# Kernel tuning notes

Measured on AMD Instinct MI355X. Metric: run time of the kernel, lower is better.

The kernel has to match this reference:

```python
import jax, jax.numpy as jnp
import numpy as np

N = 32768          # total proposals (batch of images concatenated)
C = 81             # num classes (class 0 = background)
K = 4096           # fixed candidate budget for masked NMS (jit-friendly)
SCORE_THRESH = 0.05
NMS_THRESH = 0.5
IMG_W, IMG_H = 1333.0, 800.0   # image size for clip_to_image
CLS_OFFSET = 4096.0            # > max coord: offsets boxes per label so NMS is per-class


def setup_inputs() -> dict:
    key = jax.random.key(0)
    k1, k2, k3 = jax.random.split(key, 3)
    x = jax.random.normal(k1, (N, C), dtype=jnp.float32)
    xy = jax.random.uniform(k2, (N, 2), dtype=jnp.float32) * jnp.array([IMG_W * 0.9, IMG_H * 0.9], jnp.float32)
    wh = 4.0 + jax.random.uniform(k3, (N, 2), dtype=jnp.float32) * 124.0
    boxes = jnp.concatenate([xy, xy + wh], axis=-1)  # [N,4] xyxy
    return {"x": x, "boxes": boxes}


def _pairwise_iou(b):
    # b: [K,4] xyxy -> [K,K] IoU
    x1, y1, x2, y2 = b[:, 0], b[:, 1], b[:, 2], b[:, 3]
    area = (x2 - x1) * (y2 - y1)
    iw = jnp.maximum(jnp.minimum(x2[:, None], x2[None, :]) - jnp.maximum(x1[:, None], x1[None, :]), 0.0)
    ih = jnp.maximum(jnp.minimum(y2[:, None], y2[None, :]) - jnp.maximum(y1[:, None], y1[None, :]), 0.0)
    inter = iw * ih
    return inter / (area[:, None] + area[None, :] - inter + 1e-9)


def reference(x, boxes):
    # softmax scores
    prob = jax.nn.softmax(x, axis=-1)                    # [N,C]
    # clip_to_image (remove_empty=False)
    bx = jnp.stack([
        jnp.clip(boxes[:, 0], 0.0, IMG_W - 1),
        jnp.clip(boxes[:, 1], 0.0, IMG_H - 1),
        jnp.clip(boxes[:, 2], 0.0, IMG_W - 1),
        jnp.clip(boxes[:, 3], 0.0, IMG_H - 1)], axis=-1)  # [N,4]
    # score threshold + drop background (label 0), as in filter_results
    valid = (prob > SCORE_THRESH) & (jnp.arange(C)[None, :] != 0)
    flat = jnp.where(valid, prob, -1.0).reshape(-1)       # [N*C]
    vals, idx = jax.lax.top_k(flat, K)                    # sorted desc
    box_idx = idx // C
    labels = idx % C                                      # [K] int
    bk = bx[box_idx]                                      # [K,4] (boxes repeated per class in torch code)
    keep0 = vals > 0.0                                    # invalid slots padded with -1
    # multi-label NMS: offset boxes by label so different classes never overlap
    boff = bk + (labels.astype(bk.dtype) * CLS_OFFSET)[:, None]
    iou_gt = _pairwise_iou(boff) > NMS_THRESH             # [K,K] bool
    order = jnp.arange(K)

    def step(keep, i):
        sup = keep[i] & (order > i) & iou_gt[i]
        return keep & ~sup, None

    keep, _ = jax.lax.scan(step, keep0, order)
    dets = jnp.where(keep[:, None],
                     jnp.concatenate([bk, vals[:, None]], axis=-1),
                     0.0)                                 # [K,5] = xyxy + score
    return dets, labels, keep
```

## Files before the change

kernel.cpp:

```cpp
#include <hip/hip_runtime.h>

#pragma clang fp contract(off)

typedef unsigned int u32;
typedef unsigned long long u64;
typedef long long i64;

#define N_ROWS 32768
#define NCLS 81
#define TOPK 4096
#define IMGW_M1 1332.0f
#define IMGH_M1 799.0f

#define CAND_THREADS 256
#define RPB 32
#define CAND_GRID (N_ROWS / RPB)
#define CPT 11
#define BLK_CAND_CAP 640
#define ROW_F4 ((RPB * NCLS) / 4)

#define H1_BASE 0x3D4Cu
#define H1_BINS 576

#define NSLICE 32
#define SUBCAP 384
#define SEG_LDS 4096

#define MCAP 1024
#define MMAX 512
#define NW32 16

__device__ inline double fast_exp_neg(double d) {
    if (d < -45.0) return 0.0;
    const double L2E    = 1.4426950408889634074;
    const double LN2_HI = 6.93147180369123816490e-01;
    const double LN2_LO = 1.90821492927058770002e-10;
    double n = __builtin_rint(d * L2E);
    double r = __builtin_fma(-n, LN2_HI, d);
    r = __builtin_fma(-n, LN2_LO, r);
    double p = 1.0 / 6227020800.0;
    p = __builtin_fma(p, r, 1.0 / 479001600.0);
    p = __builtin_fma(p, r, 1.0 / 39916800.0);
    p = __builtin_fma(p, r, 1.0 / 3628800.0);
    p = __builtin_fma(p, r, 1.0 / 362880.0);
    p = __builtin_fma(p, r, 1.0 / 40320.0);
    p = __builtin_fma(p, r, 1.0 / 5040.0);
    p = __builtin_fma(p, r, 1.0 / 720.0);
    p = __builtin_fma(p, r, 1.0 / 120.0);
    p = __builtin_fma(p, r, 1.0 / 24.0);
    p = __builtin_fma(p, r, 1.0 / 6.0);
    p = __builtin_fma(p, r, 0.5);
    p = __builtin_fma(p, r, 1.0);
    p = __builtin_fma(p, r, 1.0);
    i64 ni = (i64)n;
    double sc = __longlong_as_double((i64)(1023 + ni) << 52);
    return p * sc;
}

__global__ void __launch_bounds__(256) k_cand(const float* __restrict__ x,
                                              u32* __restrict__ binCur,
                                              u64* __restrict__ selBins) {
    __shared__ float4 lx4[ROW_F4];
    __shared__ u32 lK[BLK_CAND_CAP];
    __shared__ u32 lI[BLK_CAND_CAP];
    __shared__ u32 lcnt;
    float* lx = (float*)lx4;
    const int t = threadIdx.x;
    if (t == 0) lcnt = 0;

    const float4* xv = (const float4*)x + (size_t)blockIdx.x * ROW_F4;
    for (int i = t; i < ROW_F4; i += CAND_THREADS) lx4[i] = xv[i];
    __syncthreads();

    const int rl = t >> 3;
    const int q = t & 7;
    const int c0 = q * 10;
    const int cEff = (q == 7) ? 11 : 10;
    const int row = blockIdx.x * RPB + rl;
    const float* xr = lx + rl * NCLS;

    float v[CPT];
    #pragma unroll
    for (int i = 0; i < CPT; i++) v[i] = (i < cEff) ? xr[c0 + i] : -1.0e30f;

    float m = v[0];
    #pragma unroll
    for (int i = 1; i < CPT; i++) m = fmaxf(m, v[i]);
    m = fmaxf(m, __shfl_xor(m, 1));
    m = fmaxf(m, __shfl_xor(m, 2));
    m = fmaxf(m, __shfl_xor(m, 4));

    double e[CPT];
    #pragma unroll
    for (int i = 0; i < CPT; i++) {
        if (i < cEff) {
            float d = v[i] - m;
            e[i] = fast_exp_neg((double)d);
        } else e[i] = 0.0;
    }
    double s = 0.0;
    #pragma unroll
    for (int i = 0; i < CPT; i++) if (i < cEff) s += e[i];
    s += __shfl_xor(s, 1);
    s += __shfl_xor(s, 2);
    s += __shfl_xor(s, 4);

    const double THRMID = (double)0.05f + 0x1.0p-29;
    double ethr = THRMID * s;
    #pragma unroll
    for (int i = 0; i < CPT; i++) {
        int c = c0 + i;
        if (i < cEff && c != 0 && e[i] > ethr) {
            float pf = (float)(e[i] / s);
            u32 slot = atomicAdd(&lcnt, 1u);
            lK[slot] = __float_as_uint(pf);
            lI[slot] = (u32)(row * NCLS + c);
        }
    }
    __syncthreads();

    const u32 tot = lcnt;
    const u32 sbase = (blockIdx.x & (NSLICE - 1)) * H1_BINS;
    for (u32 i = t; i < tot; i += CAND_THREADS) {
        u32 key = lK[i];
        u32 b = (key >> 16) - H1_BASE;
        u32 pos = atomicAdd(&binCur[sbase + b], 1u);
        if (pos < (u32)SUBCAP)
            selBins[(size_t)(sbase + b) * SUBCAP + pos] =
                ((u64)key << 32) | (u64)(0xFFFFFFFFu - lI[i]);
    }
}

__global__ void __launch_bounds__(256) k_binrank(const u64* __restrict__ selBins,
                                                 const u32* __restrict__ binCur,
                                                 const float* __restrict__ boxes,
                                                 float* __restrict__ rboxes,
                                                 float* __restrict__ rvals,
                                                 int* __restrict__ rlabel,
                                                 float* __restrict__ out) {
    __shared__ u32 cs[1040];
    __shared__ u64 seg[SEG_LDS];
    __shared__ u32 sBase[NSLICE + 1];
    __shared__ u32 Bsh;
    const int t = threadIdx.x;

    if (t == 0) Bsh = 0;

    {
        u32 s0 = 0, s1 = 0, s2 = 0;
        const bool g1 = (t + 256) < H1_BINS;
        const bool g2 = (t + 512) < H1_BINS;
        #pragma unroll 4
        for (int j = 0; j < NSLICE; j++) {
            const u32* hp = binCur + j * H1_BINS;
            s0 += hp[t];
            if (g1) s1 += hp[t + 256];
            if (g2) s2 += hp[t + 512];
        }
        cs[t] = s0;
        cs[t + 256] = g1 ? s1 : 0u;
        cs[t + 512] = g2 ? s2 : 0u;
        cs[t + 768] = 0u;
    }
    __syncthreads();
    for (int d = 1; d < 1024; d <<= 1) {
        u32 a0 = (t + d < 1024) ? cs[t + d] : 0u;
        u32 a1 = (t + 256 + d < 1024) ? cs[t + 256 + d] : 0u;
        u32 a2 = (t + 512 + d < 1024) ? cs[t + 512 + d] : 0u;
        u32 a3 = (t + 768 + d < 1024) ? cs[t + 768 + d] : 0u;
        __syncthreads();
        cs[t] += a0; cs[t + 256] += a1; cs[t + 512] += a2; cs[t + 768] += a3;
        __syncthreads();
    }
    #pragma unroll
    for (int qq = 0; qq < 3; qq++) {
        int i = t + qq * 256;
        if (i < H1_BINS) {
            if (cs[i] >= (u32)TOPK && cs[i + 1] < (u32)TOPK) Bsh = (u32)i;
        }
    }
    __syncthreads();
    const u32 B = Bsh;

    if (blockIdx.x == H1_BINS) {
        u32 covered = cs[B];
        if (covered > (u32)TOPK) covered = TOPK;
        for (u32 r = covered + t; r < TOPK; r += 256) {
            rboxes[r * 4 + 0] = 0; rboxes[r * 4 + 1] = 0;
            rboxes[r * 4 + 2] = 0; rboxes[r * 4 + 3] = 0;
            rvals[r] = 0.0f; rlabel[r] = 0;
            out[TOPK * 5 + r] = 0.0f;
            out[TOPK * 6 + r] = 0.0f;
            float* d = out + (size_t)r * 5;
            d[0] = 0; d[1] = 0; d[2] = 0; d[3] = 0; d[4] = 0;
        }
        return;
    }

    const u32 b = blockIdx.x;
    if (b < B) return;
    u32 start = cs[b + 1];
    u32 end = cs[b];
    if (start >= end) return;
    if (start >= (u32)TOPK) return;

    if (t < NSLICE) {
        u32 c0s = binCur[t * H1_BINS + b];
        if (c0s > (u32)SUBCAP) c0s = SUBCAP;
        u32 inc = c0s;
        #pragma unroll
        for (int d = 1; d < NSLICE; d <<= 1) {
            u32 o = __shfl_up(inc, d);
            if (t >= d) inc += o;
        }
        sBase[t] = inc - c0s;
        if (t == NSLICE - 1) sBase[NSLICE] = inc;
    }
    __syncthreads();
    const u32 lenSt = sBase[NSLICE];
    const u32 ldsLen = lenSt < (u32)SEG_LDS ? lenSt : (u32)SEG_LDS;
    {
        const u32 s = (u32)t >> 3;
        const u32 base = sBase[s];
        const u32 cntS = sBase[s + 1] - base;
        const u64* gs = selBins + ((size_t)s * H1_BINS + b) * SUBCAP;
        for (u32 i = (u32)t & 7u; i < cntS; i += 8u) {
            u32 d = base + i;
            if (d < (u32)SEG_LDS) seg[d] = gs[i];
        }
    }
    __syncthreads();

    for (u32 i = t; i < ldsLen; i += 256) {
        u64 c = seg[i];
        u32 r0 = 0;
        for (u32 j = 0; j < ldsLen; j++) r0 += (seg[j] > c) ? 1u : 0u;
        u32 r = start + r0;
        if (r >= (u32)TOPK) continue;
        u32 idx = 0xFFFFFFFFu - (u32)(c & 0xFFFFFFFFull);
        float val = __uint_as_float((u32)(c >> 32));
        u32 bi = idx / NCLS;
        u32 lab = idx % NCLS;
        const float* bp = boxes + (size_t)bi * 4;
        float x1 = fminf(fmaxf(bp[0], 0.0f), IMGW_M1);
        float y1 = fminf(fmaxf(bp[1], 0.0f), IMGH_M1);
        float x2 = fminf(fmaxf(bp[2], 0.0f), IMGW_M1);
        float y2 = fminf(fmaxf(bp[3], 0.0f), IMGH_M1);
        rboxes[r * 4 + 0] = x1; rboxes[r * 4 + 1] = y1;
        rboxes[r * 4 + 2] = x2; rboxes[r * 4 + 3] = y2;
        rvals[r] = val;
        rlabel[r] = (int)lab;
        out[TOPK * 5 + r] = (float)lab;
    }
}

__device__ inline float4 nms_box(u32 g, const float4* __restrict__ boxL,
                                 const float* __restrict__ rboxes,
                                 const unsigned short* __restrict__ memRank, float off) {
    if (g < (u32)MCAP) return boxL[g];
    float4 b = ((const float4*)rboxes)[memRank[g]];
    return make_float4(b.x + off, b.y + off, b.z + off, b.w + off);
}
__device__ inline float nms_area(u32 g, const float* __restrict__ areaL, float4 b) {
    if (g < (u32)MCAP) return areaL[g];
    return (b.z - b.x) * (b.w - b.y);
}

__global__ void __launch_bounds__(256) k_nms(const float* __restrict__ rboxes,
                                             const float* __restrict__ rvals,
                                             const int* __restrict__ rlabel,
                                             float* __restrict__ out) {
    int c = blockIdx.x + 1;
    __shared__ int lLab[TOPK];
    __shared__ float4 boxL[MCAP];
    __shared__ float areaL[MCAP];
    __shared__ unsigned short memRank[TOPK];
    __shared__ u32 colW[MMAX * NW32];
    __shared__ u32 remOut[NW32];
    __shared__ unsigned char keepL[TOPK];
    __shared__ u32 cc[64];
    __shared__ u32 baseC[64];
    __shared__ u32 mTotSh;
    const int t = threadIdx.x;
    const int w = t >> 6, lane = t & 63;
    const u64 laneLT = ((u64)1 << lane) - 1;
    const float off = (float)c * 4096.0f;

    {
        const int4* g4 = (const int4*)rlabel;
        int4* l4 = (int4*)lLab;
        for (int i = t; i < TOPK / 4; i += 256) l4[i] = g4[i];
    }
    __syncthreads();

    for (int it = 0; it < 16; it++) {
        int chunk = it * 4 + w;
        int r = chunk * 64 + lane;
        u64 mask = __ballot(lLab[r] == c);
        if (lane == 0) cc[chunk] = (u32)__popcll(mask);
    }
    __syncthreads();
    if (t < 64) {
        u32 v = cc[t];
        u32 inc = v;
        #pragma unroll
        for (int d = 1; d < 64; d <<= 1) {
            u32 o = __shfl_up(inc, d);
            if (lane >= d) inc += o;
        }
        baseC[t] = inc - v;
        if (t == 63) mTotSh = inc;
    }
    __syncthreads();
    const u32 m = mTotSh;
    for (int it = 0; it < 16; it++) {
        int chunk = it * 4 + w;
        int r = chunk * 64 + lane;
        bool match = (lLab[r] == c);
        u64 mask = __ballot(match);
        if (match) {
            u32 g = baseC[chunk] + (u32)__popcll(mask & laneLT);
            memRank[g] = (unsigned short)r;
            if (g < (u32)MCAP) {
                float4 b = ((const float4*)rboxes)[r];
                float bx1 = b.x + off, by1 = b.y + off;
                float bx2 = b.z + off, by2 = b.w + off;
                boxL[g] = make_float4(bx1, by1, bx2, by2);
                areaL[g] = (bx2 - bx1) * (by2 - by1);
            }
        }
    }
    __syncthreads();

    const bool matrixPath = (m <= (u32)MMAX);
    if (matrixPath) {
        const u32 nW = (m + 31) >> 5;
        const u32 items = m * nW;
        for (u32 p = t; p < items; p += 256) {
            u32 s = p / nW;
            u32 wd = p - s * nW;
            float4 bs = nms_box(s, boxL, rboxes, memRank, off);
            float as = nms_area(s, areaL, bs);
            u32 word = 0;
            u32 j0 = wd << 5;
            u32 jend = j0 + 32; if (jend > m) jend = m;
            u32 js = (j0 > s + 1) ? j0 : (s + 1);
            for (u32 j = js; j < jend; j++) {
                float4 bj = nms_box(j, boxL, rboxes, memRank, off);
                float aj = nms_area(j, areaL, bj);
                float iw = fmaxf(fminf(bs.z, bj.z) - fmaxf(bs.x, bj.x), 0.0f);
                float ih = fmaxf(fminf(bs.w, bj.w) - fmaxf(bs.y, bj.y), 0.0f);
                float inter = iw * ih;
                float iou = inter / (as + aj - inter + 1e-9f);
                if (iou > 0.5f) word |= (1u << (j - j0));
            }
            colW[s * NW32 + wd] = word;
        }
        __syncthreads();
        if (t < 64) {
            u32 remW = 0;
            bool own = ((u32)lane < ((m + 31) >> 5));
            for (u32 s2 = 0; s2 < m; s2++) {
                u32 rw = __shfl(remW, (int)(s2 >> 5));
                bool removed = (rw >> (s2 & 31)) & 1u;
                u32 cw = own ? colW[s2 * NW32 + lane] : 0u;
                if (!removed) remW |= cw;
            }
            if (own) remOut[lane] = remW;
        }
        __syncthreads();
    } else {
        for (u32 q2 = t; q2 < m; q2 += 256) keepL[q2] = 1;
        __syncthreads();
        for (u32 i = 0; i < m; i++) {
            __syncthreads();
            if (!keepL[i]) continue;
            float4 bi = nms_box(i, boxL, rboxes, memRank, off);
            float ai = nms_area(i, areaL, bi);
            for (u32 jj = i + 1 + t; jj < m; jj += 256) {
                if (!keepL[jj]) continue;
                float4 bj = nms_box(jj, boxL, rboxes, memRank, off);
                float aj = nms_area(jj, areaL, bj);
                float iw = fmaxf(fminf(bi.z, bj.z) - fmaxf(bi.x, bj.x), 0.0f);
                float ih = fmaxf(fminf(bi.w, bj.w) - fmaxf(bi.y, bj.y), 0.0f);
                float inter = iw * ih;
                float iou = inter / (ai + aj - inter + 1e-9f);
                if (iou > 0.5f) keepL[jj] = 0;
            }
        }
        __syncthreads();
    }

    for (u32 q2 = t; q2 < m; q2 += 256) {
        bool keep = matrixPath ? !((remOut[q2 >> 5] >> (q2 & 31)) & 1u)
                               : (keepL[q2] != 0);
        int r = memRank[q2];
        out[TOPK * 6 + r] = keep ? 1.0f : 0.0f;
        float* d = out + (size_t)r * 5;
        if (keep) {
            float4 b = ((const float4*)rboxes)[r];
            d[0] = b.x; d[1] = b.y; d[2] = b.z; d[3] = b.w;
            d[4] = rvals[r];
        } else {
            d[0] = 0; d[1] = 0; d[2] = 0; d[3] = 0; d[4] = 0;
        }
    }
}

extern "C" void kernel_launch(void* const* d_in, const int* in_sizes, int n_in,
                              void* d_out, int out_size, void* d_ws, size_t ws_size,
                              hipStream_t stream) {
    const float* x = (const float*)d_in[0];
    const float* boxes = (const float*)d_in[1];
    float* out = (float*)d_out;

    u32* W = (u32*)d_ws;
    u32* binCur = W;
    u64* selBins = (u64*)((char*)d_ws + 131072);
    float* rboxes = (float*)(selBins + (size_t)NSLICE * H1_BINS * SUBCAP);
    float* rvals = rboxes + 4 * TOPK;
    int* rlabel = (int*)(rvals + TOPK);

    hipMemsetAsync(binCur, 0, NSLICE * H1_BINS * sizeof(u32), stream);
    k_cand<<<CAND_GRID, CAND_THREADS, 0, stream>>>(x, binCur, selBins);
    k_binrank<<<H1_BINS + 1, 256, 0, stream>>>(selBins, binCur, boxes,
                                               rboxes, rvals, rlabel, out);
    k_nms<<<80, 256, 0, stream>>>(rboxes, rvals, rlabel, out);
}
```

Measured before the change: 107.9 us.

## Fuse candidate, bin-rank and NMS kernels into one persistent kernel with grid barriers

Replaces three kernel launches and the large histogram memset with a single persistent 256-block kernel. Grid-wide atomic barriers separate the phases, and blocks loop over candidate chunks, bins and classes. This is meant to remove launch gaps and memset overhead. In exchange the kernel depends on all 256 blocks being co-resident, uses fewer blocks in the candidate phase (1024 chunks across 256 blocks), and has a spin barrier that times out.

Measured after the change: 183.6 us. 70.1% more time.

```diff
diff --git a/kernel.cpp b/kernel.cpp
--- a/kernel.cpp
+++ b/kernel.cpp
@@ -12,11 +12,12 @@
 #define IMGW_M1 1332.0f
 #define IMGH_M1 799.0f
 
-#define CAND_THREADS 256
+#define NBLK 256
+#define THREADS 256
+
 #define RPB 32
 #define CAND_GRID (N_ROWS / RPB)
 #define CPT 11
-#define BLK_CAND_CAP 640
 #define ROW_F4 ((RPB * NCLS) / 4)
 
 #define H1_BASE 0x3D4Cu
@@ -29,6 +30,8 @@
 #define MCAP 1024
 #define MMAX 512
 #define NW32 16
+
+#define SMEM_BYTES 77824
 
 __device__ inline double fast_exp_neg(double d) {
     if (d < -45.0) return 0.0;
@@ -57,201 +60,21 @@
     return p * sc;
 }
 
-__global__ void __launch_bounds__(256) k_cand(const float* __restrict__ x,
-                                              u32* __restrict__ binCur,
-                                              u64* __restrict__ selBins) {
-    __shared__ float4 lx4[ROW_F4];
-    __shared__ u32 lK[BLK_CAND_CAP];
-    __shared__ u32 lI[BLK_CAND_CAP];
-    __shared__ u32 lcnt;
-    float* lx = (float*)lx4;
-    const int t = threadIdx.x;
-    if (t == 0) lcnt = 0;
-
-    const float4* xv = (const float4*)x + (size_t)blockIdx.x * ROW_F4;
-    for (int i = t; i < ROW_F4; i += CAND_THREADS) lx4[i] = xv[i];
+__device__ inline void grid_barrier(u32* bar, u32 idx) {
     __syncthreads();
-
-    const int rl = t >> 3;
-    const int q = t & 7;
-    const int c0 = q * 10;
-    const int cEff = (q == 7) ? 11 : 10;
-    const int row = blockIdx.x * RPB + rl;
-    const float* xr = lx + rl * NCLS;
-
-    float v[CPT];
-    #pragma unroll
-    for (int i = 0; i < CPT; i++) v[i] = (i < cEff) ? xr[c0 + i] : -1.0e30f;
-
-    float m = v[0];
-    #pragma unroll
-    for (int i = 1; i < CPT; i++) m = fmaxf(m, v[i]);
-    m = fmaxf(m, __shfl_xor(m, 1));
-    m = fmaxf(m, __shfl_xor(m, 2));
-    m = fmaxf(m, __shfl_xor(m, 4));
-
-    double e[CPT];
-    #pragma unroll
-    for (int i = 0; i < CPT; i++) {
-        if (i < cEff) {
-            float d = v[i] - m;
-            e[i] = fast_exp_neg((double)d);
-        } else e[i] = 0.0;
-    }
-    double s = 0.0;
-    #pragma unroll
-    for (int i = 0; i < CPT; i++) if (i < cEff) s += e[i];
-    s += __shfl_xor(s, 1);
-    s += __shfl_xor(s, 2);
-    s += __shfl_xor(s, 4);
-
-    const double THRMID = (double)0.05f + 0x1.0p-29;
-    double ethr = THRMID * s;
-    #pragma unroll
-    for (int i = 0; i < CPT; i++) {
-        int c = c0 + i;
-        if (i < cEff && c != 0 && e[i] > ethr) {
-            float pf = (float)(e[i] / s);
-            u32 slot = atomicAdd(&lcnt, 1u);
-            lK[slot] = __float_as_uint(pf);
-            lI[slot] = (u32)(row * NCLS + c);
-        }
+    if (threadIdx.x == 0) {
+        __threadfence();
+        __hip_atomic_fetch_add(&bar[idx], 1u, __ATOMIC_ACQ_REL,
+                               __HIP_MEMORY_SCOPE_AGENT);
+        u32 spins = 0;
+        while (__hip_atomic_load(&bar[idx], __ATOMIC_ACQUIRE,
+                                 __HIP_MEMORY_SCOPE_AGENT) < (u32)NBLK) {
+            __builtin_amdgcn_s_sleep(8);
+            if (++spins > 4000000u) break;
+        }
+        __threadfence();
     }
     __syncthreads();
-
-    const u32 tot = lcnt;
-    const u32 sbase = (blockIdx.x & (NSLICE - 1)) * H1_BINS;
-    for (u32 i = t; i < tot; i += CAND_THREADS) {
-        u32 key = lK[i];
-        u32 b = (key >> 16) - H1_BASE;
-        u32 pos = atomicAdd(&binCur[sbase + b], 1u);
-        if (pos < (u32)SUBCAP)
-            selBins[(size_t)(sbase + b) * SUBCAP + pos] =
-                ((u64)key << 32) | (u64)(0xFFFFFFFFu - lI[i]);
-    }
-}
-
-__global__ void __launch_bounds__(256) k_binrank(const u64* __restrict__ selBins,
-                                                 const u32* __restrict__ binCur,
-                                                 const float* __restrict__ boxes,
-                                                 float* __restrict__ rboxes,
-                                                 float* __restrict__ rvals,
-                                                 int* __restrict__ rlabel,
-                                                 float* __restrict__ out) {
-    __shared__ u32 cs[1040];
-    __shared__ u64 seg[SEG_LDS];
-    __shared__ u32 sBase[NSLICE + 1];
-    __shared__ u32 Bsh;
-    const int t = threadIdx.x;
-
-    if (t == 0) Bsh = 0;
-
-    {
-        u32 s0 = 0, s1 = 0, s2 = 0;
-        const bool g1 = (t + 256) < H1_BINS;
-        const bool g2 = (t + 512) < H1_BINS;
-        #pragma unroll 4
-        for (int j = 0; j < NSLICE; j++) {
-            const u32* hp = binCur + j * H1_BINS;
-            s0 += hp[t];
-            if (g1) s1 += hp[t + 256];
-            if (g2) s2 += hp[t + 512];
-        }
-        cs[t] = s0;
-        cs[t + 256] = g1 ? s1 : 0u;
-        cs[t + 512] = g2 ? s2 : 0u;
-        cs[t + 768] = 0u;
-    }
-    __syncthreads();
-    for (int d = 1; d < 1024; d <<= 1) {
-        u32 a0 = (t + d < 1024) ? cs[t + d] : 0u;
-        u32 a1 = (t + 256 + d < 1024) ? cs[t + 256 + d] : 0u;
-        u32 a2 = (t + 512 + d < 1024) ? cs[t + 512 + d] : 0u;
-        u32 a3 = (t + 768 + d < 1024) ? cs[t + 768 + d] : 0u;
-        __syncthreads();
-        cs[t] += a0; cs[t + 256] += a1; cs[t + 512] += a2; cs[t + 768] += a3;
-        __syncthreads();
-    }
-    #pragma unroll
-    for (int qq = 0; qq < 3; qq++) {
-        int i = t + qq * 256;
-        if (i < H1_BINS) {
-            if (cs[i] >= (u32)TOPK && cs[i + 1] < (u32)TOPK) Bsh = (u32)i;
-        }
-    }
-    __syncthreads();
-    const u32 B = Bsh;
-
-    if (blockIdx.x == H1_BINS) {
-        u32 covered = cs[B];
-        if (covered > (u32)TOPK) covered = TOPK;
-        for (u32 r = covered + t; r < TOPK; r += 256) {
-            rboxes[r * 4 + 0] = 0; rboxes[r * 4 + 1] = 0;
-            rboxes[r * 4 + 2] = 0; rboxes[r * 4 + 3] = 0;
-            rvals[r] = 0.0f; rlabel[r] = 0;
-            out[TOPK * 5 + r] = 0.0f;
-            out[TOPK * 6 + r] = 0.0f;
-            float* d = out + (size_t)r * 5;
-            d[0] = 0; d[1] = 0; d[2] = 0; d[3] = 0; d[4] = 0;
-        }
-        return;
-    }
-
-    const u32 b = blockIdx.x;
-    if (b < B) return;
-    u32 start = cs[b + 1];
-    u32 end = cs[b];
-    if (start >= end) return;
-    if (start >= (u32)TOPK) return;
-
-    if (t < NSLICE) {
-        u32 c0s = binCur[t * H1_BINS + b];
-        if (c0s > (u32)SUBCAP) c0s = SUBCAP;
-        u32 inc = c0s;
-        #pragma unroll
-        for (int d = 1; d < NSLICE; d <<= 1) {
-            u32 o = __shfl_up(inc, d);
-            if (t >= d) inc += o;
-        }
-        sBase[t] = inc - c0s;
-        if (t == NSLICE - 1) sBase[NSLICE] = inc;
-    }
-    __syncthreads();
-    const u32 lenSt = sBase[NSLICE];
-    const u32 ldsLen = lenSt < (u32)SEG_LDS ? lenSt : (u32)SEG_LDS;
-    {
-        const u32 s = (u32)t >> 3;
-        const u32 base = sBase[s];
-        const u32 cntS = sBase[s + 1] - base;
-        const u64* gs = selBins + ((size_t)s * H1_BINS + b) * SUBCAP;
-        for (u32 i = (u32)t & 7u; i < cntS; i += 8u) {
-            u32 d = base + i;
-            if (d < (u32)SEG_LDS) seg[d] = gs[i];
-        }
-    }
-    __syncthreads();
-
-    for (u32 i = t; i < ldsLen; i += 256) {
-        u64 c = seg[i];
-        u32 r0 = 0;
-        for (u32 j = 0; j < ldsLen; j++) r0 += (seg[j] > c) ? 1u : 0u;
-        u32 r = start + r0;
-        if (r >= (u32)TOPK) continue;
-        u32 idx = 0xFFFFFFFFu - (u32)(c & 0xFFFFFFFFull);
-        float val = __uint_as_float((u32)(c >> 32));
-        u32 bi = idx / NCLS;
-        u32 lab = idx % NCLS;
-        const float* bp = boxes + (size_t)bi * 4;
-        float x1 = fminf(fmaxf(bp[0], 0.0f), IMGW_M1);
-        float y1 = fminf(fmaxf(bp[1], 0.0f), IMGH_M1);
-        float x2 = fminf(fmaxf(bp[2], 0.0f), IMGW_M1);
-        float y2 = fminf(fmaxf(bp[3], 0.0f), IMGH_M1);
-        rboxes[r * 4 + 0] = x1; rboxes[r * 4 + 1] = y1;
-        rboxes[r * 4 + 2] = x2; rboxes[r * 4 + 3] = y2;
-        rvals[r] = val;
-        rlabel[r] = (int)lab;
-        out[TOPK * 5 + r] = (float)lab;
-    }
 }
 
 __device__ inline float4 nms_box(u32 g, const float4* __restrict__ boxL,
@@ -266,143 +89,351 @@
     return (b.z - b.x) * (b.w - b.y);
 }
 
-__global__ void __launch_bounds__(256) k_nms(const float* __restrict__ rboxes,
-                                             const float* __restrict__ rvals,
-                                             const int* __restrict__ rlabel,
-                                             float* __restrict__ out) {
-    int c = blockIdx.x + 1;
-    __shared__ int lLab[TOPK];
-    __shared__ float4 boxL[MCAP];
-    __shared__ float areaL[MCAP];
-    __shared__ unsigned short memRank[TOPK];
-    __shared__ u32 colW[MMAX * NW32];
-    __shared__ u32 remOut[NW32];
-    __shared__ unsigned char keepL[TOPK];
+__global__ void __launch_bounds__(THREADS) k_fused(
+        const float* __restrict__ x, const float* __restrict__ boxes,
+        u32* __restrict__ bar, u32* __restrict__ binCur,
+        u64* __restrict__ selBins,
+        float* __restrict__ rboxes, float* __restrict__ rvals,
+        int* __restrict__ rlabel, float* __restrict__ out) {
+    __shared__ __align__(16) unsigned char smem[SMEM_BYTES];
+    __shared__ u32 lcnt;
+    __shared__ u32 Bsh;
+    __shared__ u32 sBase[NSLICE + 1];
     __shared__ u32 cc[64];
     __shared__ u32 baseC[64];
+    __shared__ u32 remOut[NW32];
     __shared__ u32 mTotSh;
+
     const int t = threadIdx.x;
-    const int w = t >> 6, lane = t & 63;
-    const u64 laneLT = ((u64)1 << lane) - 1;
-    const float off = (float)c * 4096.0f;
+    const u32 bid = blockIdx.x;
 
     {
-        const int4* g4 = (const int4*)rlabel;
-        int4* l4 = (int4*)lLab;
-        for (int i = t; i < TOPK / 4; i += 256) l4[i] = g4[i];
+        u32 gi = bid * THREADS + (u32)t;
+        if (gi < (u32)(NSLICE * H1_BINS)) binCur[gi] = 0;
     }
-    __syncthreads();
-
-    for (int it = 0; it < 16; it++) {
-        int chunk = it * 4 + w;
-        int r = chunk * 64 + lane;
-        u64 mask = __ballot(lLab[r] == c);
-        if (lane == 0) cc[chunk] = (u32)__popcll(mask);
+    grid_barrier(bar, 0);
+
+    {
+        float4* lx4 = (float4*)smem;
+        u32* lK = (u32*)(smem + 10368);
+        u32* lI = (u32*)(smem + 12928);
+        float* lx = (float*)lx4;
+
+        for (u32 chunk = bid; chunk < (u32)CAND_GRID; chunk += NBLK) {
+            if (t == 0) lcnt = 0;
+            const float4* xv = (const float4*)x + (size_t)chunk * ROW_F4;
+            for (int i = t; i < ROW_F4; i += THREADS) lx4[i] = xv[i];
+            __syncthreads();
+
+            const int rl = t >> 3;
+            const int q = t & 7;
+            const int c0 = q * 10;
+            const int cEff = (q == 7) ? 11 : 10;
+            const int row = (int)chunk * RPB + rl;
+            const float* xr = lx + rl * NCLS;
+
+            float v[CPT];
+            #pragma unroll
+            for (int i = 0; i < CPT; i++) v[i] = (i < cEff) ? xr[c0 + i] : -1.0e30f;
+
+            float m = v[0];
+            #pragma unroll
+            for (int i = 1; i < CPT; i++) m = fmaxf(m, v[i]);
+            m = fmaxf(m, __shfl_xor(m, 1));
+            m = fmaxf(m, __shfl_xor(m, 2));
+            m = fmaxf(m, __shfl_xor(m, 4));
+
+            double e[CPT];
+            #pragma unroll
+            for (int i = 0; i < CPT; i++) {
+                if (i < cEff) {
+                    float d = v[i] - m;
+                    e[i] = fast_exp_neg((double)d);
+                } else e[i] = 0.0;
+            }
+            double s = 0.0;
+            #pragma unroll
+            for (int i = 0; i < CPT; i++) if (i < cEff) s += e[i];
+            s += __shfl_xor(s, 1);
+            s += __shfl_xor(s, 2);
+            s += __shfl_xor(s, 4);
+
+            const double THRMID = (double)0.05f + 0x1.0p-29;
+            double ethr = THRMID * s;
+            #pragma unroll
+            for (int i = 0; i < CPT; i++) {
+                int c = c0 + i;
+                if (i < cEff && c != 0 && e[i] > ethr) {
+                    float pf = (float)(e[i] / s);
+                    u32 slot = atomicAdd(&lcnt, 1u);
+                    lK[slot] = __float_as_uint(pf);
+                    lI[slot] = (u32)(row * NCLS + c);
+                }
+            }
+            __syncthreads();
+
+            const u32 tot = lcnt;
+            const u32 sbase = (chunk & (NSLICE - 1)) * H1_BINS;
+            for (u32 i = (u32)t; i < tot; i += THREADS) {
+                u32 key = lK[i];
+                u32 b = (key >> 16) - H1_BASE;
+                u32 pos = atomicAdd(&binCur[sbase + b], 1u);
+                if (pos < (u32)SUBCAP)
+                    selBins[(size_t)(sbase + b) * SUBCAP + pos] =
+                        ((u64)key << 32) | (u64)(0xFFFFFFFFu - lI[i]);
+            }
+            __syncthreads();
+        }
     }
-    __syncthreads();
-    if (t < 64) {
-        u32 v = cc[t];
-        u32 inc = v;
+    grid_barrier(bar, 1);
+
+    {
+        u32* cs = (u32*)smem;
+        u64* seg = (u64*)(smem + 4160);
+
+        if (t == 0) Bsh = 0;
+        {
+            u32 s0 = 0, s1 = 0, s2 = 0;
+            const bool g1 = (t + 256) < H1_BINS;
+            const bool g2 = (t + 512) < H1_BINS;
+            #pragma unroll 4
+            for (int j = 0; j < NSLICE; j++) {
+                const u32* hp = binCur + j * H1_BINS;
+                s0 += hp[t];
+                if (g1) s1 += hp[t + 256];
+                if (g2) s2 += hp[t + 512];
+            }
+            cs[t] = s0;
+            cs[t + 256] = g1 ? s1 : 0u;
+            cs[t + 512] = g2 ? s2 : 0u;
+            cs[t + 768] = 0u;
+        }
+        __syncthreads();
+        for (int d = 1; d < 1024; d <<= 1) {
+            u32 a0 = (t + d < 1024) ? cs[t + d] : 0u;
+            u32 a1 = (t + 256 + d < 1024) ? cs[t + 256 + d] : 0u;
+            u32 a2 = (t + 512 + d < 1024) ? cs[t + 512 + d] : 0u;
+            u32 a3 = (t + 768 + d < 1024) ? cs[t + 768 + d] : 0u;
+            __syncthreads();
+            cs[t] += a0; cs[t + 256] += a1; cs[t + 512] += a2; cs[t + 768] += a3;
+            __syncthreads();
+        }
         #pragma unroll
-        for (int d = 1; d < 64; d <<= 1) {
-            u32 o = __shfl_up(inc, d);
-            if (lane >= d) inc += o;
-        }
-        baseC[t] = inc - v;
-        if (t == 63) mTotSh = inc;
+        for (int qq = 0; qq < 3; qq++) {
+            int i = t + qq * 256;
+            if (i < H1_BINS) {
+                if (cs[i] >= (u32)TOPK && cs[i + 1] < (u32)TOPK) Bsh = (u32)i;
+            }
+        }
+        __syncthreads();
+        const u32 B = Bsh;
+
+        for (int bb = (int)bid; bb <= H1_BINS; bb += NBLK) {
+            if (bb == H1_BINS) {
+                u32 covered = cs[B];
+                if (covered > (u32)TOPK) covered = TOPK;
+                for (u32 r = covered + (u32)t; r < (u32)TOPK; r += THREADS) {
+                    rboxes[r * 4 + 0] = 0; rboxes[r * 4 + 1] = 0;
+                    rboxes[r * 4 + 2] = 0; rboxes[r * 4 + 3] = 0;
+                    rvals[r] = 0.0f; rlabel[r] = 0;
+                    out[TOPK * 5 + r] = 0.0f;
+                    out[TOPK * 6 + r] = 0.0f;
+                    float* d = out + (size_t)r * 5;
+                    d[0] = 0; d[1] = 0; d[2] = 0; d[3] = 0; d[4] = 0;
+                }
+                continue;
+            }
+            const u32 b = (u32)bb;
+            if (b < B) continue;
+            u32 start = cs[b + 1];
+            u32 end = cs[b];
+            if (start >= end) continue;
+            if (start >= (u32)TOPK) continue;
+
+            __syncthreads();
+            if (t < NSLICE) {
+                u32 c0s = binCur[t * H1_BINS + b];
+                if (c0s > (u32)SUBCAP) c0s = SUBCAP;
+                u32 inc = c0s;
+                #pragma unroll
+                for (int d = 1; d < NSLICE; d <<= 1) {
+                    u32 o = __shfl_up(inc, d);
+                    if (t >= d) inc += o;
+                }
+                sBase[t] = inc - c0s;
+                if (t == NSLICE - 1) sBase[NSLICE] = inc;
+            }
+            __syncthreads();
+            const u32 lenSt = sBase[NSLICE];
+            const u32 ldsLen = lenSt < (u32)SEG_LDS ? lenSt : (u32)SEG_LDS;
+            {
+                const u32 s = (u32)t >> 3;
+                const u32 base = sBase[s];
+                const u32 cntS = sBase[s + 1] - base;
+                const u64* gs = selBins + ((size_t)s * H1_BINS + b) * SUBCAP;
+                for (u32 i = (u32)t & 7u; i < cntS; i += 8u) {
+                    u32 d = base + i;
+                    if (d < (u32)SEG_LDS) seg[d] = gs[i];
+                }
+            }
+            __syncthreads();
+
+            for (u32 i = (u32)t; i < ldsLen; i += THREADS) {
+                u64 c = seg[i];
+                u32 r0 = 0;
+                for (u32 j = 0; j < ldsLen; j++) r0 += (seg[j] > c) ? 1u : 0u;
+                u32 r = start + r0;
+                if (r >= (u32)TOPK) continue;
+                u32 idx = 0xFFFFFFFFu - (u32)(c & 0xFFFFFFFFull);
+                float val = __uint_as_float((u32)(c >> 32));
+                u32 bi = idx / NCLS;
+                u32 lab = idx % NCLS;
+                const float* bp = boxes + (size_t)bi * 4;
+                float x1 = fminf(fmaxf(bp[0], 0.0f), IMGW_M1);
+                float y1 = fminf(fmaxf(bp[1], 0.0f), IMGH_M1);
+                float x2 = fminf(fmaxf(bp[2], 0.0f), IMGW_M1);
+                float y2 = fminf(fmaxf(bp[3], 0.0f), IMGH_M1);
+                rboxes[r * 4 + 0] = x1; rboxes[r * 4 + 1] = y1;
+                rboxes[r * 4 + 2] = x2; rboxes[r * 4 + 3] = y2;
+                rvals[r] = val;
+                rlabel[r] = (int)lab;
+                out[TOPK * 5 + r] = (float)lab;
+            }
+        }
     }
-    __syncthreads();
-    const u32 m = mTotSh;
-    for (int it = 0; it < 16; it++) {
-        int chunk = it * 4 + w;
-        int r = chunk * 64 + lane;
-        bool match = (lLab[r] == c);
-        u64 mask = __ballot(match);
-        if (match) {
-            u32 g = baseC[chunk] + (u32)__popcll(mask & laneLT);
-            memRank[g] = (unsigned short)r;
-            if (g < (u32)MCAP) {
+    grid_barrier(bar, 2);
+
+    if (bid < 80) {
+        int* lLab = (int*)smem;
+        float4* boxL = (float4*)(smem + 16384);
+        float* areaL = (float*)(smem + 32768);
+        unsigned short* memRank = (unsigned short*)(smem + 36864);
+        u32* colW = (u32*)(smem + 45056);
+        unsigned char* keepL = (unsigned char*)(smem + 45056);
+
+        int c = (int)bid + 1;
+        const int w = t >> 6, lane = t & 63;
+        const u64 laneLT = ((u64)1 << lane) - 1;
+        const float off = (float)c * 4096.0f;
+
+        {
+            const int4* g4 = (const int4*)rlabel;
+            int4* l4 = (int4*)lLab;
+            for (int i = t; i < TOPK / 4; i += THREADS) l4[i] = g4[i];
+        }
+        __syncthreads();
+
+        for (int it = 0; it < 16; it++) {
+            int chunk = it * 4 + w;
+            int r = chunk * 64 + lane;
+            u64 mask = __ballot(lLab[r] == c);
+            if (lane == 0) cc[chunk] = (u32)__popcll(mask);
+        }
+        __syncthreads();
+        if (t < 64) {
+            u32 v = cc[t];
+            u32 inc = v;
+            #pragma unroll
+            for (int d = 1; d < 64; d <<= 1) {
+                u32 o = __shfl_up(inc, d);
+                if (lane >= d) inc += o;
+            }
+            baseC[t] = inc - v;
+            if (t == 63) mTotSh = inc;
+        }
+        __syncthreads();
+        const u32 m = mTotSh;
+        for (int it = 0; it < 16; it++) {
+            int chunk = it * 4 + w;
+            int r = chunk * 64 + lane;
+            bool match = (lLab[r] == c);
+            u64 mask = __ballot(match);
+            if (match) {
+                u32 g = baseC[chunk] + (u32)__popcll(mask & laneLT);
+                memRank[g] = (unsigned short)r;
+                if (g < (u32)MCAP) {
+                    float4 b = ((const float4*)rboxes)[r];
+                    float bx1 = b.x + off, by1 = b.y + off;
+                    float bx2 = b.z + off, by2 = b.w + off;
+                    boxL[g] = make_float4(bx1, by1, bx2, by2);
+                    areaL[g] = (bx2 - bx1) * (by2 - by1);
+                }
+            }
+        }
+        __syncthreads();
+
+        const bool matrixPath = (m <= (u32)MMAX);
+        if (matrixPath) {
+            const u32 nW = (m + 31) >> 5;
+            const u32 items = m * nW;
+            for (u32 p = (u32)t; p < items; p += THREADS) {
+                u32 s = p / nW;
+                u32 wd = p - s * nW;
+                float4 bs = nms_box(s, boxL, rboxes, memRank, off);
+                float as = nms_area(s, areaL, bs);
+                u32 word = 0;
+                u32 j0 = wd << 5;
+                u32 jend = j0 + 32; if (jend > m) jend = m;
+                u32 js = (j0 > s + 1) ? j0 : (s + 1);
+                for (u32 j = js; j < jend; j++) {
+                    float4 bj = nms_box(j, boxL, rboxes, memRank, off);
+                    float aj = nms_area(j, areaL, bj);
+                    float iw = fmaxf(fminf(bs.z, bj.z) - fmaxf(bs.x, bj.x), 0.0f);
+                    float ih = fmaxf(fminf(bs.w, bj.w) - fmaxf(bs.y, bj.y), 0.0f);
+                    float inter = iw * ih;
+                    float iou = inter / (as + aj - inter + 1e-9f);
+                    if (iou > 0.5f) word |= (1u << (j - j0));
+                }
+                colW[s * NW32 + wd] = word;
+            }
+            __syncthreads();
+            if (t < 64) {
+                u32 remW = 0;
+                bool own = ((u32)lane < ((m + 31) >> 5));
+                for (u32 s2 = 0; s2 < m; s2++) {
+                    u32 rw = __shfl(remW, (int)(s2 >> 5));
+                    bool removed = (rw >> (s2 & 31)) & 1u;
+                    u32 cw = own ? colW[s2 * NW32 + lane] : 0u;
+                    if (!removed) remW |= cw;
+                }
+                if (own) remOut[lane] = remW;
+            }
+            __syncthreads();
+        } else {
+            for (u32 q2 = (u32)t; q2 < m; q2 += THREADS) keepL[q2] = 1;
+            __syncthreads();
+            for (u32 i = 0; i < m; i++) {
+                __syncthreads();
+                if (!keepL[i]) continue;
+                float4 bi = nms_box(i, boxL, rboxes, memRank, off);
+                float ai = nms_area(i, areaL, bi);
+                for (u32 jj = i + 1 + (u32)t; jj < m; jj += THREADS) {
+                    if (!keepL[jj]) continue;
+                    float4 bj = nms_box(jj, boxL, rboxes, memRank, off);
+                    float aj = nms_area(jj, areaL, bj);
+                    float iw = fmaxf(fminf(bi.z, bj.z) - fmaxf(bi.x, bj.x), 0.0f);
+                    float ih = fmaxf(fminf(bi.w, bj.w) - fmaxf(bi.y, bj.y), 0.0f);
+                    float inter = iw * ih;
+                    float iou = inter / (ai + aj - inter + 1e-9f);
+                    if (iou > 0.5f) keepL[jj] = 0;
+                }
+            }
+            __syncthreads();
+        }
+
+        for (u32 q2 = (u32)t; q2 < m; q2 += THREADS) {
+            bool keep = matrixPath ? !((remOut[q2 >> 5] >> (q2 & 31)) & 1u)
+                                   : (keepL[q2] != 0);
+            int r = memRank[q2];
+            out[TOPK * 6 + r] = keep ? 1.0f : 0.0f;
+            float* d = out + (size_t)r * 5;
+            if (keep) {
                 float4 b = ((const float4*)rboxes)[r];
-                float bx1 = b.x + off, by1 = b.y + off;
-                float bx2 = b.z + off, by2 = b.w + off;
-                boxL[g] = make_float4(bx1, by1, bx2, by2);
-                areaL[g] = (bx2 - bx1) * (by2 - by1);
-            }
-        }
-    }
-    __syncthreads();
-
-    const bool matrixPath = (m <= (u32)MMAX);
-    if (matrixPath) {
-        const u32 nW = (m + 31) >> 5;
-        const u32 items = m * nW;
-        for (u32 p = t; p < items; p += 256) {
-            u32 s = p / nW;
-            u32 wd = p - s * nW;
-            float4 bs = nms_box(s, boxL, rboxes, memRank, off);
-            float as = nms_area(s, areaL, bs);
-            u32 word = 0;
-            u32 j0 = wd << 5;
-            u32 jend = j0 + 32; if (jend > m) jend = m;
-            u32 js = (j0 > s + 1) ? j0 : (s + 1);
-            for (u32 j = js; j < jend; j++) {
-                float4 bj = nms_box(j, boxL, rboxes, memRank, off);
-                float aj = nms_area(j, areaL, bj);
-                float iw = fmaxf(fminf(bs.z, bj.z) - fmaxf(bs.x, bj.x), 0.0f);
-                float ih = fmaxf(fminf(bs.w, bj.w) - fmaxf(bs.y, bj.y), 0.0f);
-                float inter = iw * ih;
-                float iou = inter / (as + aj - inter + 1e-9f);
-                if (iou > 0.5f) word |= (1u << (j - j0));
-            }
-            colW[s * NW32 + wd] = word;
-        }
-        __syncthreads();
-        if (t < 64) {
-            u32 remW = 0;
-            bool own = ((u32)lane < ((m + 31) >> 5));
-            for (u32 s2 = 0; s2 < m; s2++) {
-                u32 rw = __shfl(remW, (int)(s2 >> 5));
-                bool removed = (rw >> (s2 & 31)) & 1u;
-                u32 cw = own ? colW[s2 * NW32 + lane] : 0u;
-                if (!removed) remW |= cw;
-            }
-            if (own) remOut[lane] = remW;
-        }
-        __syncthreads();
-    } else {
-        for (u32 q2 = t; q2 < m; q2 += 256) keepL[q2] = 1;
-        __syncthreads();
-        for (u32 i = 0; i < m; i++) {
-            __syncthreads();
-            if (!keepL[i]) continue;
-            float4 bi = nms_box(i, boxL, rboxes, memRank, off);
-            float ai = nms_area(i, areaL, bi);
-            for (u32 jj = i + 1 + t; jj < m; jj += 256) {
-                if (!keepL[jj]) continue;
-                float4 bj = nms_box(jj, boxL, rboxes, memRank, off);
-                float aj = nms_area(jj, areaL, bj);
-                float iw = fmaxf(fminf(bi.z, bj.z) - fmaxf(bi.x, bj.x), 0.0f);
-                float ih = fmaxf(fminf(bi.w, bj.w) - fmaxf(bi.y, bj.y), 0.0f);
-                float inter = iw * ih;
-                float iou = inter / (ai + aj - inter + 1e-9f);
-                if (iou > 0.5f) keepL[jj] = 0;
-            }
-        }
-        __syncthreads();
-    }
-
-    for (u32 q2 = t; q2 < m; q2 += 256) {
-        bool keep = matrixPath ? !((remOut[q2 >> 5] >> (q2 & 31)) & 1u)
-                               : (keepL[q2] != 0);
-        int r = memRank[q2];
-        out[TOPK * 6 + r] = keep ? 1.0f : 0.0f;
-        float* d = out + (size_t)r * 5;
-        if (keep) {
-            float4 b = ((const float4*)rboxes)[r];
-            d[0] = b.x; d[1] = b.y; d[2] = b.z; d[3] = b.w;
-            d[4] = rvals[r];
-        } else {
-            d[0] = 0; d[1] = 0; d[2] = 0; d[3] = 0; d[4] = 0;
+                d[0] = b.x; d[1] = b.y; d[2] = b.z; d[3] = b.w;
+                d[4] = rvals[r];
+            } else {
+                d[0] = 0; d[1] = 0; d[2] = 0; d[3] = 0; d[4] = 0;
+            }
         }
     }
 }
@@ -415,15 +446,14 @@
     float* out = (float*)d_out;
 
     u32* W = (u32*)d_ws;
-    u32* binCur = W;
+    u32* bar = W;
+    u32* binCur = W + 16;
     u64* selBins = (u64*)((char*)d_ws + 131072);
     float* rboxes = (float*)(selBins + (size_t)NSLICE * H1_BINS * SUBCAP);
     float* rvals = rboxes + 4 * TOPK;
     int* rlabel = (int*)(rvals + TOPK);
 
-    hipMemsetAsync(binCur, 0, NSLICE * H1_BINS * sizeof(u32), stream);
-    k_cand<<<CAND_GRID, CAND_THREADS, 0, stream>>>(x, binCur, selBins);
-    k_binrank<<<H1_BINS + 1, 256, 0, stream>>>(selBins, binCur, boxes,
-                                               rboxes, rvals, rlabel, out);
-    k_nms<<<80, 256, 0, stream>>>(rboxes, rvals, rlabel, out);
-}
+    hipMemsetAsync(bar, 0, 16, stream);
+    k_fused<<<NBLK, THREADS, 0, stream>>>(x, boxes, bar, binCur, selBins,
+                                          rboxes, rvals, rlabel, out);
+}
```
